# Performance work log

Hardware: AMD Instinct MI355X
Metric: run time of the kernel (lower is better)

## Reference

```python
import jax, jax.numpy as jnp
import numpy as np

B, T, N, F, H, E = 8, 24, 4000, 32, 128, 64000


def setup_inputs() -> dict:
    key = jax.random.key(0)
    ks = jax.random.split(key, 8)
    s = lambda k, shape: jax.random.normal(k, shape, jnp.float32) * 0.05
    return {
        "dynamic_features": jax.random.normal(ks[0], (B, T, N, F), jnp.float32),
        "edge_index": jax.random.randint(ks[1], (2, E), 0, N),
        "W_ih": s(ks[2], (4 * H, F)),
        "W_hh": s(ks[3], (4 * H, H)),
        "b_ih": jnp.zeros((4 * H,), jnp.float32),
        "b_hh": jnp.zeros((4 * H,), jnp.float32),
        "gcn_W": s(ks[4], (H, H)),
        "gcn_b": jnp.zeros((H,), jnp.float32),
        "fc_count_w": s(ks[5], (1, H)),
        "fc_count_b": jnp.zeros((1,), jnp.float32),
        "fc_income_w": s(ks[6], (1, H)),
        "fc_income_b": jnp.zeros((1,), jnp.float32),
    }


def _lstm_last(x, W_ih, W_hh, b_ih, b_hh):
    # x: [M, T, F] -> last hidden state [M, H]; PyTorch gate order (i, f, g, o)
    M = x.shape[0]
    Hh = W_hh.shape[1]
    xg = jnp.einsum('mtf,gf->mtg', x, W_ih) + b_ih + b_hh  # [M, T, 4H]

    def step(carry, xt):
        h, c = carry
        g = xt + h @ W_hh.T
        i, f, gg, o = jnp.split(g, 4, axis=-1)
        i = jax.nn.sigmoid(i)
        f = jax.nn.sigmoid(f)
        gg = jnp.tanh(gg)
        o = jax.nn.sigmoid(o)
        c = f * c + i * gg
        h = o * jnp.tanh(c)
        return (h, c), None

    h0 = jnp.zeros((M, Hh), x.dtype)
    (h, _), _ = jax.lax.scan(step, (h0, h0), jnp.swapaxes(xg, 0, 1))
    return h


def reference(dynamic_features, edge_index, W_ih, W_hh, b_ih, b_hh,
              gcn_W, gcn_b, fc_count_w, fc_count_b, fc_income_w, fc_income_b):
    b, t, n, f = dynamic_features.shape
    Hh = W_hh.shape[1]

    # temporal encoding: [B, T, N, F] -> [B*N, T, F] -> last hidden [B, N, H]
    lstm_in = dynamic_features.transpose(0, 2, 1, 3).reshape(b * n, t, f)
    h = _lstm_last(lstm_in, W_ih, W_hh, b_ih, b_hh).reshape(b, n, Hh)

    # PyG GCNConv norm: add self-loops, deg^{-1/2} on both ends
    loops = jnp.arange(n)
    src = jnp.concatenate([edge_index[0], loops])
    dst = jnp.concatenate([edge_index[1], loops])
    deg = jax.ops.segment_sum(jnp.ones_like(src, jnp.float32), dst, num_segments=n)
    dinv = jnp.where(deg > 0, deg ** -0.5, 0.0)
    norm = dinv[src] * dinv[dst]  # [E+N]

    def gcn_relu(xb):  # xb: [N, H]
        xw = xb @ gcn_W.T
        msg = xw[src] * norm[:, None]
        agg = jax.ops.segment_sum(msg, dst, num_segments=n) + gcn_b
        return jax.nn.relu(agg)

    gcn_out = jax.vmap(gcn_relu)(h)  # [B, N, H]

    count_pred = (gcn_out @ fc_count_w.T + fc_count_b).reshape(b, n)
    income_pred = (gcn_out @ fc_income_w.T + fc_income_b).reshape(b, n)
    return count_pred, income_pred
```

## Files before the change

kernel.cpp:

```cpp
#include <hip/hip_runtime.h>

#define NB 8
#define TT 24
#define NN 4000
#define FF 32
#define HH 128
#define EE 64000

typedef float f32x4 __attribute__((ext_vector_type(4)));
typedef short bf16x8 __attribute__((ext_vector_type(8)));
#define MFMA16(a, b, c) __builtin_amdgcn_mfma_f32_16x16x32_bf16(a, b, c, 0, 0, 0)

__device__ __forceinline__ float fsig(float x) {
  return __builtin_amdgcn_rcpf(1.0f + __expf(-x));
}
__device__ __forceinline__ float ftanh(float x) {
  return 1.0f - 2.0f * __builtin_amdgcn_rcpf(__expf(2.0f * x) + 1.0f);
}

__device__ __forceinline__ unsigned short rne16(float x, float* hif) {
  unsigned u = __float_as_uint(x);
  unsigned r = (u + 0x7FFFu + ((u >> 16) & 1u)) >> 16;
  *hif = __uint_as_float(r << 16);
  return (unsigned short)r;
}

__device__ __forceinline__ unsigned rnd_top(float x) {
  unsigned u = __float_as_uint(x);
  return u + 0x7FFFu + ((u >> 16) & 1u);
}

__global__ __launch_bounds__(256) void setup_xsplit_kernel(
    const float* __restrict__ x, const float* __restrict__ W_ih, const float* __restrict__ W_hh,
    const float* __restrict__ b_ih, const float* __restrict__ b_hh,
    const float* __restrict__ gcn_W,
    unsigned short* __restrict__ Wbh_hi, unsigned short* __restrict__ Wbh_lo,
    unsigned short* __restrict__ Wbi_hi, unsigned short* __restrict__ Wbi_lo,
    float* __restrict__ gcn_WT, float* __restrict__ bias,
    int* __restrict__ ecnt, int* __restrict__ fillc,
    unsigned short* __restrict__ xpk) {
  if (blockIdx.x < 418) {
    int idx = blockIdx.x * 256 + threadIdx.x;
    if (idx < 65536) {
      int e = idx & 7, l = (idx >> 3) & 63, ks = (idx >> 9) & 3, nt = idx >> 11;
      int gate = nt * 16 + (l & 15);
      int k = ks * 32 + (l >> 4) * 8 + e;
      float wv = W_hh[gate * 128 + k];
      float hif, d;
      unsigned short hb = rne16(wv, &hif);
      unsigned short lb = rne16(wv - hif, &d);
      Wbh_hi[idx] = hb;
      Wbh_lo[idx] = lb;
    } else if (idx < 65536 + 16384) {
      int p = idx - 65536;
      int e = p & 7, l = (p >> 3) & 63, nt = p >> 9;
      int gate = nt * 16 + (l & 15);
      int k = (l >> 4) * 8 + e;
      float wv = W_ih[gate * 32 + k];
      float hif, d;
      unsigned short hb = rne16(wv, &hif);
      unsigned short lb = rne16(wv - hif, &d);
      Wbi_hi[p] = hb;
      Wbi_lo[p] = lb;
    } else if (idx < 65536 + 16384 + 16384) {
      int p = idx - 65536 - 16384;
      int g = p & 127, k = p >> 7;
      gcn_WT[p] = gcn_W[g * 128 + k];
    } else if (idx < 65536 + 16384 + 16384 + 512) {
      int g = idx - (65536 + 16384 + 16384);
      bias[g] = b_ih[g] + b_hh[g];
    } else if (idx < 65536 + 16384 + 16384 + 512 + NN) {
      ecnt[idx - (65536 + 16384 + 16384 + 512)] = 0;
    } else if (idx < 65536 + 16384 + 16384 + 512 + 2 * NN) {
      fillc[idx - (65536 + 16384 + 16384 + 512 + NN)] = 0;
    }
  } else {
    int gid = (blockIdx.x - 418) * 256 + threadIdx.x;
    int l = gid & 63;
    int t = (gid >> 6) % TT;
    int rt = gid / (TT * 64);
    int col = l & 15, kc = l >> 4;
    int r = rt * 16 + col;
    int b = (rt * 16) / NN;
    int n = r - b * NN;
    const float* src = x + (((size_t)b * TT + t) * NN + n) * FF + kc * 8;
    float4 p0 = *(const float4*)src;
    float4 p1 = *(const float4*)(src + 4);
    float xf[8] = {p0.x, p0.y, p0.z, p0.w, p1.x, p1.y, p1.z, p1.w};
    bf16x8 vh, vl;
#pragma unroll
    for (int e = 0; e < 8; ++e) {
      float hif, d;
      vh[e] = (short)rne16(xf[e], &hif);
      vl[e] = (short)rne16(xf[e] - hif, &d);
    }
    size_t ob = (size_t)(rt * TT + t) * 1024 + l * 8;
    *(bf16x8*)(xpk + ob) = vh;
    *(bf16x8*)(xpk + ob + 512) = vl;
  }
}

__global__ __launch_bounds__(256) void lstm_kernel(
    const unsigned short* __restrict__ xpk,
    const unsigned short* __restrict__ Wbh_hi, const unsigned short* __restrict__ Wbh_lo,
    const unsigned short* __restrict__ Wbi_hi, const unsigned short* __restrict__ Wbi_lo,
    const float* __restrict__ bias,
    float* __restrict__ h_out) {
  __shared__ unsigned short hbuf[2][2][32 * 128];
  const int tid = threadIdx.x;
  const int w = tid >> 6, l = tid & 63;
  const int col = l & 15, kc = l >> 4;
  const int blk = blockIdx.x;

  {
    uint4* p0 = (uint4*)&hbuf[0][0][0];
    for (int i = tid; i < 1024; i += 256) p0[i] = make_uint4(0, 0, 0, 0);
  }

  float c[2][2][4];
#pragma unroll
  for (int sq = 0; sq < 2; ++sq)
#pragma unroll
    for (int u = 0; u < 2; ++u)
#pragma unroll
      for (int r = 0; r < 4; ++r) c[sq][u][r] = 0.0f;

  __syncthreads();

  for (int t = 0; t < TT; ++t) {
    const char* hr_hi = (const char*)&hbuf[t & 1][0][0];
    const char* hr_lo = (const char*)&hbuf[t & 1][1][0];
    char* hw_hi = (char*)&hbuf[(t + 1) & 1][0][0];
    char* hw_lo = (char*)&hbuf[(t + 1) & 1][1][0];

    bf16x8 xh[2], xl[2];
#pragma unroll
    for (int sq = 0; sq < 2; ++sq) {
      const unsigned short* xb = xpk + ((size_t)(blk * 2 + sq) * TT + t) * 1024 + l * 8;
      xh[sq] = *(const bf16x8*)xb;
      xl[sq] = *(const bf16x8*)(xb + 512);
    }

    f32x4 acc[2][8];

    __builtin_amdgcn_s_setprio(1);
#pragma unroll
    for (int ks = 0; ks < 4; ++ks) {
      bf16x8 bh[2], bl_[2];
#pragma unroll
      for (int sq = 0; sq < 2; ++sq) {
        int off = (16 * sq + col) * 256 + (((4 * ks + kc) ^ col) << 4);
        bh[sq] = *(const bf16x8*)(hr_hi + off);
        bl_[sq] = *(const bf16x8*)(hr_lo + off);
      }
#pragma unroll
      for (int q = 0; q < 8; ++q) {
        size_t wo = ((size_t)((4 * q + w) * 4 + ks) * 64 + l) * 8;
        bf16x8 wh = *(const bf16x8*)(Wbh_hi + wo);
        bf16x8 wl = *(const bf16x8*)(Wbh_lo + wo);
        f32x4 cseed;
        if (ks == 0)
          cseed = *(const f32x4*)(bias + (q >> 1) * 128 + ((q & 1) * 4 + w) * 16 + 4 * kc);
#pragma unroll
        for (int sq = 0; sq < 2; ++sq) {
          acc[sq][q] = MFMA16(wh, bh[sq], ks == 0 ? cseed : acc[sq][q]);
          acc[sq][q] = MFMA16(wh, bl_[sq], acc[sq][q]);
          acc[sq][q] = MFMA16(wl, bh[sq], acc[sq][q]);
        }
      }
    }
#pragma unroll
    for (int q = 0; q < 8; ++q) {
      size_t wo = ((size_t)(4 * q + w) * 64 + l) * 8;
      bf16x8 wh = *(const bf16x8*)(Wbi_hi + wo);
      bf16x8 wl = *(const bf16x8*)(Wbi_lo + wo);
#pragma unroll
      for (int sq = 0; sq < 2; ++sq) {
        acc[sq][q] = MFMA16(wh, xh[sq], acc[sq][q]);
        acc[sq][q] = MFMA16(wh, xl[sq], acc[sq][q]);
        acc[sq][q] = MFMA16(wl, xh[sq], acc[sq][q]);
      }
    }
    __builtin_amdgcn_s_setprio(0);

#pragma unroll
    for (int u = 0; u < 2; ++u) {
      int jb = w + 4 * u;
#pragma unroll
      for (int sq = 0; sq < 2; ++sq) {
        unsigned uh[4], ul[4];
        float hv[4];
#pragma unroll
        for (int r = 0; r < 4; ++r) {
          float iv = fsig(acc[sq][0 + u][r]);
          float fv = fsig(acc[sq][2 + u][r]);
          float gv = ftanh(acc[sq][4 + u][r]);
          float ov = fsig(acc[sq][6 + u][r]);
          float cc = fv * c[sq][u][r] + iv * gv;
          c[sq][u][r] = cc;
          float hh = ov * ftanh(cc);
          hv[r] = hh;
          unsigned uu = __float_as_uint(hh);
          uh[r] = uu;
          float hif = __uint_as_float(uu & 0xFFFF0000u);
          ul[r] = rnd_top(hh - hif);
        }
        uint2 phi, plo;
        phi.x = __builtin_amdgcn_perm(uh[1], uh[0], 0x07060302u);
        phi.y = __builtin_amdgcn_perm(uh[3], uh[2], 0x07060302u);
        plo.x = __builtin_amdgcn_perm(ul[1], ul[0], 0x07060302u);
        plo.y = __builtin_amdgcn_perm(ul[3], ul[2], 0x07060302u);
        int row = 16 * sq + col;
        int cs = (2 * jb + (kc >> 1)) ^ col;
        int woff = row * 256 + cs * 16 + 8 * (kc & 1);
        *(uint2*)(hw_hi + woff) = phi;
        *(uint2*)(hw_lo + woff) = plo;
        if (t == TT - 1) {
          int rowg = blk * 32 + 16 * sq + col;
          *(float4*)&h_out[(size_t)rowg * HH + 16 * jb + 4 * kc] =
              make_float4(hv[0], hv[1], hv[2], hv[3]);
        }
      }
    }
    __syncthreads();
  }
}

__global__ void hist_kernel(const int* __restrict__ ei, int* __restrict__ ecnt) {
  int e = blockIdx.x * 256 + threadIdx.x;
  if (e < EE) atomicAdd(&ecnt[ei[EE + e]], 1);
}

__global__ __launch_bounds__(1024) void scan_kernel(const int* __restrict__ ecnt,
                                                    int* __restrict__ rowptr,
                                                    float* __restrict__ dinv) {
  __shared__ int s[4096];
  int tid = threadIdx.x;
  for (int i = tid; i < 4096; i += 1024) {
    int v = (i < NN) ? ecnt[i] : 0;
    s[i] = v;
    if (i < NN) dinv[i] = 1.0f / sqrtf((float)v + 1.0f);
  }
  __syncthreads();
  for (int off = 1; off < 4096; off <<= 1) {
    int v[4];
#pragma unroll
    for (int k = 0; k < 4; ++k) {
      int i = tid + k * 1024;
      v[k] = s[i] + ((i >= off) ? s[i - off] : 0);
    }
    __syncthreads();
#pragma unroll
    for (int k = 0; k < 4; ++k) s[tid + k * 1024] = v[k];
    __syncthreads();
  }
  for (int i = tid; i <= NN; i += 1024) rowptr[i] = (i == 0) ? 0 : s[i - 1];
}

__global__ void fill_kernel(const int* __restrict__ ei, const float* __restrict__ dinv,
                            const int* __restrict__ rowptr, int* __restrict__ fillc,
                            int2* __restrict__ epk) {
  int e = blockIdx.x * 256 + threadIdx.x;
  if (e >= EE) return;
  int s = ei[e], d = ei[EE + e];
  int pos = rowptr[d] + atomicAdd(&fillc[d], 1);
  float nrm = dinv[s] * dinv[d];
  epk[pos] = make_int2(s, __float_as_int(nrm));
}

__global__ __launch_bounds__(128) void xw_kernel(const float* __restrict__ h,
                                                 const float* __restrict__ gcn_WT,
                                                 float* __restrict__ xw) {
  const int r0 = blockIdx.x * 8;
  const int g = threadIdx.x;
  __shared__ float hs[8][HH];
  for (int m = 0; m < 8; ++m) hs[m][g] = h[(size_t)(r0 + m) * HH + g];
  __syncthreads();
  float acc[8] = {0, 0, 0, 0, 0, 0, 0, 0};
#pragma unroll 4
  for (int k = 0; k < HH; ++k) {
    float w = gcn_WT[k * HH + g];
#pragma unroll
    for (int m = 0; m < 8; ++m) acc[m] += hs[m][k] * w;
  }
  for (int m = 0; m < 8; ++m) xw[(size_t)(r0 + m) * HH + g] = acc[m];
}

__global__ __launch_bounds__(128) void gather_final_kernel(
    const float* __restrict__ xw, const float* __restrict__ dinv,
    const int* __restrict__ rowptr, const int2* __restrict__ epk,
    const float* __restrict__ gcn_b,
    const float* __restrict__ fcw_c, const float* __restrict__ fcb_c,
    const float* __restrict__ fcw_i, const float* __restrict__ fcb_i,
    float* __restrict__ out) {
  const int d = blockIdx.x;
  const int j = threadIdx.x;
  float acc[NB];
#pragma unroll
  for (int b = 0; b < NB; ++b) acc[b] = 0.0f;
  const int p0 = rowptr[d], p1 = rowptr[d + 1];
  for (int p = p0; p < p1; ++p) {
    int2 ep = epk[p];
    int s = ep.x;
    float nrm = __int_as_float(ep.y);
#pragma unroll
    for (int b = 0; b < NB; ++b)
      acc[b] += xw[((size_t)b * NN + s) * HH + j] * nrm;
  }
  float sn = dinv[d] * dinv[d];
  float bj = gcn_b[j], wc = fcw_c[j], wi = fcw_i[j];
  __shared__ float red[2][NB][2];
  int lane = j & 63, wv = j >> 6;
#pragma unroll
  for (int b = 0; b < NB; ++b) {
    float v = acc[b] + xw[((size_t)b * NN + d) * HH + j] * sn + bj;
    v = fmaxf(v, 0.0f);
    float sc = v * wc, si = v * wi;
#pragma unroll
    for (int off = 32; off > 0; off >>= 1) {
      sc += __shfl_down(sc, off);
      si += __shfl_down(si, off);
    }
    if (lane == 0) {
      red[wv][b][0] = sc;
      red[wv][b][1] = si;
    }
  }
  __syncthreads();
  if (j < NB) {
    out[(size_t)j * NN + d] = red[0][j][0] + red[1][j][0] + fcb_c[0];
    out[(size_t)(NB + j) * NN + d] = red[0][j][1] + red[1][j][1] + fcb_i[0];
  }
}

extern "C" void kernel_launch(void* const* d_in, const int* in_sizes, int n_in,
                              void* d_out, int out_size, void* d_ws, size_t ws_size,
                              hipStream_t stream) {
  const float* x     = (const float*)d_in[0];
  const int*   ei    = (const int*)d_in[1];
  const float* W_ih  = (const float*)d_in[2];
  const float* W_hh  = (const float*)d_in[3];
  const float* b_ih  = (const float*)d_in[4];
  const float* b_hh  = (const float*)d_in[5];
  const float* gcn_W = (const float*)d_in[6];
  const float* gcn_b = (const float*)d_in[7];
  const float* fcw_c = (const float*)d_in[8];
  const float* fcb_c = (const float*)d_in[9];
  const float* fcw_i = (const float*)d_in[10];
  const float* fcb_i = (const float*)d_in[11];
  float* out = (float*)d_out;

  char* cur = (char*)d_ws;
  unsigned short* Wbh_hi = (unsigned short*)cur; cur += 65536 * 2;
  unsigned short* Wbh_lo = (unsigned short*)cur; cur += 65536 * 2;
  unsigned short* Wbi_hi = (unsigned short*)cur; cur += 16384 * 2;
  unsigned short* Wbi_lo = (unsigned short*)cur; cur += 16384 * 2;
  float* gcn_WT = (float*)cur; cur += 16384 * 4;
  float* bias   = (float*)cur; cur += 512 * 4;
  float* dinv   = (float*)cur; cur += 4096 * 4;
  int*   ecnt   = (int*)cur;   cur += 4096 * 4;
  int*   fillc  = (int*)cur;   cur += 4096 * 4;
  int*   rowptr = (int*)cur;   cur += 8192 * 4;
  int2*  epk    = (int2*)cur;  cur += (size_t)EE * 8;
  float* h_all  = (float*)cur; cur += (size_t)4096000 * 4;
  unsigned short* xpk = (unsigned short*)cur;
  float* xw = (float*)cur;

  setup_xsplit_kernel<<<12418, 256, 0, stream>>>(x, W_ih, W_hh, b_ih, b_hh, gcn_W,
                                                 Wbh_hi, Wbh_lo, Wbi_hi, Wbi_lo,
                                                 gcn_WT, bias, ecnt, fillc, xpk);
  lstm_kernel<<<(NB * NN) / 32, 256, 0, stream>>>(xpk, Wbh_hi, Wbh_lo, Wbi_hi, Wbi_lo,
                                                  bias, h_all);
  hist_kernel<<<EE / 256, 256, 0, stream>>>(ei, ecnt);
  scan_kernel<<<1, 1024, 0, stream>>>(ecnt, rowptr, dinv);
  fill_kernel<<<EE / 256, 256, 0, stream>>>(ei, dinv, rowptr, fillc, epk);
  xw_kernel<<<(NB * NN) / 8, 128, 0, stream>>>(h_all, gcn_WT, xw);
  gather_final_kernel<<<NN, 128, 0, stream>>>(xw, dinv, rowptr, epk, gcn_b,
                                              fcw_c, fcb_c, fcw_i, fcb_i, out);
}
```

Before: 461.6 us.

## Split LSTM gate accumulation into two halves and target two blocks per CU

The per-timestep gate GEMM is restructured so each wave computes accumulators for one half of its hidden columns (4 gate tiles) at a time, then applies the LSTM cell update before starting the other half, instead of holding all 8 tiles at once. This halves live accumulator registers, and launch_bounds now requests 2 blocks per CU to raise occupancy. The trade-off is reloading the h tile fragments from LDS twice per step and less MFMA back-to-back work per phase, in exchange for better latency hiding across waves.

```diff
diff --git a/kernel.cpp b/kernel.cpp
--- a/kernel.cpp
+++ b/kernel.cpp
@@ -100,7 +100,7 @@
   }
 }
 
-__global__ __launch_bounds__(256) void lstm_kernel(
+__global__ __launch_bounds__(256, 2) void lstm_kernel(
     const unsigned short* __restrict__ xpk,
     const unsigned short* __restrict__ Wbh_hi, const unsigned short* __restrict__ Wbh_lo,
     const unsigned short* __restrict__ Wbi_hi, const unsigned short* __restrict__ Wbi_lo,
@@ -141,50 +141,52 @@
       xl[sq] = *(const bf16x8*)(xb + 512);
     }
 
-    f32x4 acc[2][8];
-
-    __builtin_amdgcn_s_setprio(1);
-#pragma unroll
-    for (int ks = 0; ks < 4; ++ks) {
-      bf16x8 bh[2], bl_[2];
-#pragma unroll
-      for (int sq = 0; sq < 2; ++sq) {
-        int off = (16 * sq + col) * 256 + (((4 * ks + kc) ^ col) << 4);
-        bh[sq] = *(const bf16x8*)(hr_hi + off);
-        bl_[sq] = *(const bf16x8*)(hr_lo + off);
+#pragma unroll
+    for (int u = 0; u < 2; ++u) {
+      f32x4 acc[2][4];
+
+      __builtin_amdgcn_s_setprio(1);
+#pragma unroll
+      for (int ks = 0; ks < 4; ++ks) {
+        bf16x8 bh[2], bl_[2];
+#pragma unroll
+        for (int sq = 0; sq < 2; ++sq) {
+          int off = (16 * sq + col) * 256 + (((4 * ks + kc) ^ col) << 4);
+          bh[sq] = *(const bf16x8*)(hr_hi + off);
+          bl_[sq] = *(const bf16x8*)(hr_lo + off);
+        }
+#pragma unroll
+        for (int g = 0; g < 4; ++g) {
+          int nt = 8 * g + 4 * u + w;
+          size_t wo = ((size_t)(nt * 4 + ks) * 64 + l) * 8;
+          bf16x8 wh = *(const bf16x8*)(Wbh_hi + wo);
+          bf16x8 wl = *(const bf16x8*)(Wbh_lo + wo);
+          f32x4 cseed;
+          if (ks == 0)
+            cseed = *(const f32x4*)(bias + g * 128 + (4 * u + w) * 16 + 4 * kc);
+#pragma unroll
+          for (int sq = 0; sq < 2; ++sq) {
+            acc[sq][g] = MFMA16(wh, bh[sq], ks == 0 ? cseed : acc[sq][g]);
+            acc[sq][g] = MFMA16(wh, bl_[sq], acc[sq][g]);
+            acc[sq][g] = MFMA16(wl, bh[sq], acc[sq][g]);
+          }
+        }
       }
 #pragma unroll
-      for (int q = 0; q < 8; ++q) {
-        size_t wo = ((size_t)((4 * q + w) * 4 + ks) * 64 + l) * 8;
-        bf16x8 wh = *(const bf16x8*)(Wbh_hi + wo);
-        bf16x8 wl = *(const bf16x8*)(Wbh_lo + wo);
-        f32x4 cseed;
-        if (ks == 0)
-          cseed = *(const f32x4*)(bias + (q >> 1) * 128 + ((q & 1) * 4 + w) * 16 + 4 * kc);
+      for (int g = 0; g < 4; ++g) {
+        int nt = 8 * g + 4 * u + w;
+        size_t wo = ((size_t)nt * 64 + l) * 8;
+        bf16x8 wh = *(const bf16x8*)(Wbi_hi + wo);
+        bf16x8 wl = *(const bf16x8*)(Wbi_lo + wo);
 #pragma unroll
         for (int sq = 0; sq < 2; ++sq) {
-          acc[sq][q] = MFMA16(wh, bh[sq], ks == 0 ? cseed : acc[sq][q]);
-          acc[sq][q] = MFMA16(wh, bl_[sq], acc[sq][q]);
-          acc[sq][q] = MFMA16(wl, bh[sq], acc[sq][q]);
+          acc[sq][g] = MFMA16(wh, xh[sq], acc[sq][g]);
+          acc[sq][g] = MFMA16(wh, xl[sq], acc[sq][g]);
+          acc[sq][g] = MFMA16(wl, xh[sq], acc[sq][g]);
         }
       }
-    }
-#pragma unroll
-    for (int q = 0; q < 8; ++q) {
-      size_t wo = ((size_t)(4 * q + w) * 64 + l) * 8;
-      bf16x8 wh = *(const bf16x8*)(Wbi_hi + wo);
-      bf16x8 wl = *(const bf16x8*)(Wbi_lo + wo);
-#pragma unroll
-      for (int sq = 0; sq < 2; ++sq) {
-        acc[sq][q] = MFMA16(wh, xh[sq], acc[sq][q]);
-        acc[sq][q] = MFMA16(wh, xl[sq], acc[sq][q]);
-        acc[sq][q] = MFMA16(wl, xh[sq], acc[sq][q]);
-      }
-    }
-    __builtin_amdgcn_s_setprio(0);
-
-#pragma unroll
-    for (int u = 0; u < 2; ++u) {
+      __builtin_amdgcn_s_setprio(0);
+
       int jb = w + 4 * u;
 #pragma unroll
       for (int sq = 0; sq < 2; ++sq) {
@@ -192,10 +194,10 @@
         float hv[4];
 #pragma unroll
         for (int r = 0; r < 4; ++r) {
-          float iv = fsig(acc[sq][0 + u][r]);
-          float fv = fsig(acc[sq][2 + u][r]);
-          float gv = ftanh(acc[sq][4 + u][r]);
-          float ov = fsig(acc[sq][6 + u][r]);
+          float iv = fsig(acc[sq][0][r]);
+          float fv = fsig(acc[sq][1][r]);
+          float gv = ftanh(acc[sq][2][r]);
+          float ov = fsig(acc[sq][3][r]);
           float cc = fv * c[sq][u][r] + iv * gv;
           c[sq][u][r] = cc;
           float hh = ov * ftanh(cc);
```

Result: slower. 1.003 ms (+117.3%).

## Stream LSTM weight tiles into LDS with double-buffered async global_load_lds

Applied to the files above, without the earlier changes.

Replaces the per-step direct global loads of the recurrent and input weight fragments with a per-wave double-buffered prefetch pipeline. Each iteration uses global_load_lds to stage the next two gate tiles into LDS, waits with an explicit vmcnt, then reads the current tiles from LDS for the MFMAs. The aim is to hide L2 latency on weight fetches behind MFMA work. It also drops the s_setprio hints. It adds LDS traffic and extra waits, and the hand-written vmcnt depends on the compiler not reordering other global loads.

```diff
diff --git a/kernel.cpp b/kernel.cpp
--- a/kernel.cpp
+++ b/kernel.cpp
@@ -10,6 +10,10 @@
 typedef float f32x4 __attribute__((ext_vector_type(4)));
 typedef short bf16x8 __attribute__((ext_vector_type(8)));
 #define MFMA16(a, b, c) __builtin_amdgcn_mfma_f32_16x16x32_bf16(a, b, c, 0, 0, 0)
+
+typedef const __attribute__((address_space(1))) unsigned int* gas1_t;
+typedef __attribute__((address_space(3))) unsigned int* las3_t;
+#define DMA16(g, s) __builtin_amdgcn_global_load_lds((gas1_t)(g), (las3_t)(s), 16, 0, 0)
 
 __device__ __forceinline__ float fsig(float x) {
   return __builtin_amdgcn_rcpf(1.0f + __expf(-x));
@@ -107,6 +111,7 @@
     const float* __restrict__ bias,
     float* __restrict__ h_out) {
   __shared__ unsigned short hbuf[2][2][32 * 128];
+  __shared__ unsigned short wbuf[4][2][2048];
   const int tid = threadIdx.x;
   const int w = tid >> 6, l = tid & 63;
   const int col = l & 15, kc = l >> 4;
@@ -126,6 +131,14 @@
       for (int r = 0; r < 4; ++r) c[sq][u][r] = 0.0f;
 
   __syncthreads();
+
+#define HHOFF(q, ks) ((size_t)(((4 * (q) + w) * 4 + (ks)) * 512) + l * 8)
+#define IHOFF(q) ((size_t)((4 * (q) + w) * 512) + l * 8)
+
+  DMA16(Wbh_hi + HHOFF(0, 0), &wbuf[w][0][0]);
+  DMA16(Wbh_lo + HHOFF(0, 0), &wbuf[w][0][512]);
+  DMA16(Wbh_hi + HHOFF(1, 0), &wbuf[w][0][1024]);
+  DMA16(Wbh_lo + HHOFF(1, 0), &wbuf[w][0][1536]);
 
   for (int t = 0; t < TT; ++t) {
     const char* hr_hi = (const char*)&hbuf[t & 1][0][0];
@@ -143,7 +156,6 @@
 
     f32x4 acc[2][8];
 
-    __builtin_amdgcn_s_setprio(1);
 #pragma unroll
     for (int ks = 0; ks < 4; ++ks) {
       bf16x8 bh[2], bl_[2];
@@ -154,34 +166,79 @@
         bl_[sq] = *(const bf16x8*)(hr_lo + off);
       }
 #pragma unroll
-      for (int q = 0; q < 8; ++q) {
-        size_t wo = ((size_t)((4 * q + w) * 4 + ks) * 64 + l) * 8;
-        bf16x8 wh = *(const bf16x8*)(Wbh_hi + wo);
-        bf16x8 wl = *(const bf16x8*)(Wbh_lo + wo);
-        f32x4 cseed;
-        if (ks == 0)
-          cseed = *(const f32x4*)(bias + (q >> 1) * 128 + ((q & 1) * 4 + w) * 16 + 4 * kc);
+      for (int j = 0; j < 4; ++j) {
+        const int m = ks * 4 + j;
+        const int cpar = m & 1, npar = cpar ^ 1;
+        if (m + 1 < 16) {
+          const int nks = (m + 1) >> 2, nj = (m + 1) & 3;
+          const int nq0 = 2 * nj, nq1 = 2 * nj + 1;
+          DMA16(Wbh_hi + HHOFF(nq0, nks), &wbuf[w][npar][0]);
+          DMA16(Wbh_lo + HHOFF(nq0, nks), &wbuf[w][npar][512]);
+          DMA16(Wbh_hi + HHOFF(nq1, nks), &wbuf[w][npar][1024]);
+          DMA16(Wbh_lo + HHOFF(nq1, nks), &wbuf[w][npar][1536]);
+        } else {
+          DMA16(Wbi_hi + IHOFF(0), &wbuf[w][npar][0]);
+          DMA16(Wbi_lo + IHOFF(0), &wbuf[w][npar][512]);
+          DMA16(Wbi_hi + IHOFF(1), &wbuf[w][npar][1024]);
+          DMA16(Wbi_lo + IHOFF(1), &wbuf[w][npar][1536]);
+        }
+        asm volatile("s_waitcnt vmcnt(4)" ::: "memory");
+        const unsigned short* wb = &wbuf[w][cpar][0];
+        bf16x8 wh0 = *(const bf16x8*)(wb + l * 8);
+        bf16x8 wl0 = *(const bf16x8*)(wb + 512 + l * 8);
+        bf16x8 wh1 = *(const bf16x8*)(wb + 1024 + l * 8);
+        bf16x8 wl1 = *(const bf16x8*)(wb + 1536 + l * 8);
+        const int q0 = 2 * j, q1 = 2 * j + 1;
+        f32x4 cs0, cs1;
+        if (ks == 0) {
+          cs0 = *(const f32x4*)(bias + (q0 >> 1) * 128 + ((q0 & 1) * 4 + w) * 16 + 4 * kc);
+          cs1 = *(const f32x4*)(bias + (q1 >> 1) * 128 + ((q1 & 1) * 4 + w) * 16 + 4 * kc);
+        }
 #pragma unroll
         for (int sq = 0; sq < 2; ++sq) {
-          acc[sq][q] = MFMA16(wh, bh[sq], ks == 0 ? cseed : acc[sq][q]);
-          acc[sq][q] = MFMA16(wh, bl_[sq], acc[sq][q]);
-          acc[sq][q] = MFMA16(wl, bh[sq], acc[sq][q]);
+          acc[sq][q0] = MFMA16(wh0, bh[sq], ks == 0 ? cs0 : acc[sq][q0]);
+          acc[sq][q0] = MFMA16(wh0, bl_[sq], acc[sq][q0]);
+          acc[sq][q0] = MFMA16(wl0, bh[sq], acc[sq][q0]);
+          acc[sq][q1] = MFMA16(wh1, bh[sq], ks == 0 ? cs1 : acc[sq][q1]);
+          acc[sq][q1] = MFMA16(wh1, bl_[sq], acc[sq][q1]);
+          acc[sq][q1] = MFMA16(wl1, bh[sq], acc[sq][q1]);
         }
       }
     }
-#pragma unroll
-    for (int q = 0; q < 8; ++q) {
-      size_t wo = ((size_t)(4 * q + w) * 64 + l) * 8;
-      bf16x8 wh = *(const bf16x8*)(Wbi_hi + wo);
-      bf16x8 wl = *(const bf16x8*)(Wbi_lo + wo);
+
+#pragma unroll
+    for (int j = 0; j < 4; ++j) {
+      const int m = 16 + j;
+      const int cpar = m & 1, npar = cpar ^ 1;
+      if (j < 3) {
+        const int nq0 = 2 * (j + 1), nq1 = nq0 + 1;
+        DMA16(Wbi_hi + IHOFF(nq0), &wbuf[w][npar][0]);
+        DMA16(Wbi_lo + IHOFF(nq0), &wbuf[w][npar][512]);
+        DMA16(Wbi_hi + IHOFF(nq1), &wbuf[w][npar][1024]);
+        DMA16(Wbi_lo + IHOFF(nq1), &wbuf[w][npar][1536]);
+      } else {
+        DMA16(Wbh_hi + HHOFF(0, 0), &wbuf[w][npar][0]);
+        DMA16(Wbh_lo + HHOFF(0, 0), &wbuf[w][npar][512]);
+        DMA16(Wbh_hi + HHOFF(1, 0), &wbuf[w][npar][1024]);
+        DMA16(Wbh_lo + HHOFF(1, 0), &wbuf[w][npar][1536]);
+      }
+      asm volatile("s_waitcnt vmcnt(4)" ::: "memory");
+      const unsigned short* wb = &wbuf[w][cpar][0];
+      bf16x8 wh0 = *(const bf16x8*)(wb + l * 8);
+      bf16x8 wl0 = *(const bf16x8*)(wb + 512 + l * 8);
+      bf16x8 wh1 = *(const bf16x8*)(wb + 1024 + l * 8);
+      bf16x8 wl1 = *(const bf16x8*)(wb + 1536 + l * 8);
+      const int q0 = 2 * j, q1 = 2 * j + 1;
 #pragma unroll
       for (int sq = 0; sq < 2; ++sq) {
-        acc[sq][q] = MFMA16(wh, xh[sq], acc[sq][q]);
-        acc[sq][q] = MFMA16(wh, xl[sq], acc[sq][q]);
-        acc[sq][q] = MFMA16(wl, xh[sq], acc[sq][q]);
+        acc[sq][q0] = MFMA16(wh0, xh[sq], acc[sq][q0]);
+        acc[sq][q0] = MFMA16(wh0, xl[sq], acc[sq][q0]);
+        acc[sq][q0] = MFMA16(wl0, xh[sq], acc[sq][q0]);
+        acc[sq][q1] = MFMA16(wh1, xh[sq], acc[sq][q1]);
+        acc[sq][q1] = MFMA16(wh1, xl[sq], acc[sq][q1]);
+        acc[sq][q1] = MFMA16(wl1, xh[sq], acc[sq][q1]);
       }
     }
-    __builtin_amdgcn_s_setprio(0);
 
 #pragma unroll
     for (int u = 0; u < 2; ++u) {
@@ -224,6 +281,8 @@
     }
     __syncthreads();
   }
+#undef HHOFF
+#undef IHOFF
 }
 
 __global__ void hist_kernel(const int* __restrict__ ei, int* __restrict__ ecnt) {
```

After: 637.6 us. 38.1% more time.

## Stream LSTM weights through double-buffered LDS via async global_load_lds

Applied to the files above, without the earlier changes.

Replaces direct global loads of the recurrent and input weight fragments in the LSTM time loop with asynchronous global-to-LDS DMA copies, issued one phase ahead into a per-wave double buffer. Weights are consumed from LDS, and the wait is expressed as a manual vmcnt count. The goal is to hide global/L2 latency behind the MFMA work. In exchange it adds 64KB of LDS per block, which can cut occupancy, and drops the s_setprio hints. The hand-coded vmcnt accounting is fragile because the xpk and bias global loads share that counter.

```diff
diff --git a/kernel.cpp b/kernel.cpp
--- a/kernel.cpp
+++ b/kernel.cpp
@@ -10,6 +10,10 @@
 typedef float f32x4 __attribute__((ext_vector_type(4)));
 typedef short bf16x8 __attribute__((ext_vector_type(8)));
 #define MFMA16(a, b, c) __builtin_amdgcn_mfma_f32_16x16x32_bf16(a, b, c, 0, 0, 0)
+
+typedef const __attribute__((address_space(1))) unsigned int* gas1_t;
+typedef __attribute__((address_space(3))) unsigned int* las3_t;
+#define DMA16(g, s) __builtin_amdgcn_global_load_lds((gas1_t)(g), (las3_t)(s), 16, 0, 0)
 
 __device__ __forceinline__ float fsig(float x) {
   return __builtin_amdgcn_rcpf(1.0f + __expf(-x));
@@ -107,6 +111,7 @@
     const float* __restrict__ bias,
     float* __restrict__ h_out) {
   __shared__ unsigned short hbuf[2][2][32 * 128];
+  __shared__ unsigned short wbuf[4][2][8][512];
   const int tid = threadIdx.x;
   const int w = tid >> 6, l = tid & 63;
   const int col = l & 15, kc = l >> 4;
@@ -126,6 +131,25 @@
       for (int r = 0; r < 4; ++r) c[sq][u][r] = 0.0f;
 
   __syncthreads();
+
+#define STAGE(p, par)                                                              \
+  {                                                                                \
+    _Pragma("unroll") for (int s = 0; s < 8; ++s) {                                \
+      const unsigned short* srcp;                                                  \
+      if ((p) < 8) {                                                               \
+        int q = 4 * ((p) & 1) + (s >> 1);                                          \
+        size_t off = (size_t)(((4 * q + w) * 4 + ((p) >> 1)) * 512) + l * 8;       \
+        srcp = ((s & 1) ? Wbh_lo : Wbh_hi) + off;                                  \
+      } else {                                                                     \
+        int q = 4 * ((p) - 8) + (s >> 1);                                          \
+        size_t off = (size_t)((4 * q + w) * 512) + l * 8;                          \
+        srcp = ((s & 1) ? Wbi_lo : Wbi_hi) + off;                                  \
+      }                                                                            \
+      DMA16(srcp, &wbuf[w][par][s][0]);                                            \
+    }                                                                              \
+  }
+
+  STAGE(0, 0);
 
   for (int t = 0; t < TT; ++t) {
     const char* hr_hi = (const char*)&hbuf[t & 1][0][0];
@@ -133,55 +157,68 @@
     char* hw_hi = (char*)&hbuf[(t + 1) & 1][0][0];
     char* hw_lo = (char*)&hbuf[(t + 1) & 1][1][0];
 
+    f32x4 acc[2][8];
     bf16x8 xh[2], xl[2];
-#pragma unroll
-    for (int sq = 0; sq < 2; ++sq) {
-      const unsigned short* xb = xpk + ((size_t)(blk * 2 + sq) * TT + t) * 1024 + l * 8;
-      xh[sq] = *(const bf16x8*)xb;
-      xl[sq] = *(const bf16x8*)(xb + 512);
-    }
-
-    f32x4 acc[2][8];
-
-    __builtin_amdgcn_s_setprio(1);
-#pragma unroll
-    for (int ks = 0; ks < 4; ++ks) {
-      bf16x8 bh[2], bl_[2];
-#pragma unroll
-      for (int sq = 0; sq < 2; ++sq) {
-        int off = (16 * sq + col) * 256 + (((4 * ks + kc) ^ col) << 4);
-        bh[sq] = *(const bf16x8*)(hr_hi + off);
-        bl_[sq] = *(const bf16x8*)(hr_lo + off);
+
+#pragma unroll
+    for (int p = 0; p < 10; ++p) {
+      const int cpar = p & 1, npar = cpar ^ 1;
+      if (p < 9) {
+        STAGE(p + 1, npar);
+      } else {
+        STAGE(0, npar);
       }
-#pragma unroll
-      for (int q = 0; q < 8; ++q) {
-        size_t wo = ((size_t)((4 * q + w) * 4 + ks) * 64 + l) * 8;
-        bf16x8 wh = *(const bf16x8*)(Wbh_hi + wo);
-        bf16x8 wl = *(const bf16x8*)(Wbh_lo + wo);
-        f32x4 cseed;
-        if (ks == 0)
-          cseed = *(const f32x4*)(bias + (q >> 1) * 128 + ((q & 1) * 4 + w) * 16 + 4 * kc);
+      asm volatile("s_waitcnt vmcnt(8)" ::: "memory");
+
+      if (p == 0) {
 #pragma unroll
         for (int sq = 0; sq < 2; ++sq) {
-          acc[sq][q] = MFMA16(wh, bh[sq], ks == 0 ? cseed : acc[sq][q]);
-          acc[sq][q] = MFMA16(wh, bl_[sq], acc[sq][q]);
-          acc[sq][q] = MFMA16(wl, bh[sq], acc[sq][q]);
+          const unsigned short* xb = xpk + ((size_t)(blk * 2 + sq) * TT + t) * 1024 + l * 8;
+          xh[sq] = *(const bf16x8*)xb;
+          xl[sq] = *(const bf16x8*)(xb + 512);
         }
       }
-    }
-#pragma unroll
-    for (int q = 0; q < 8; ++q) {
-      size_t wo = ((size_t)(4 * q + w) * 64 + l) * 8;
-      bf16x8 wh = *(const bf16x8*)(Wbi_hi + wo);
-      bf16x8 wl = *(const bf16x8*)(Wbi_lo + wo);
-#pragma unroll
-      for (int sq = 0; sq < 2; ++sq) {
-        acc[sq][q] = MFMA16(wh, xh[sq], acc[sq][q]);
-        acc[sq][q] = MFMA16(wh, xl[sq], acc[sq][q]);
-        acc[sq][q] = MFMA16(wl, xh[sq], acc[sq][q]);
+
+      const unsigned short* wb = &wbuf[w][cpar][0][0];
+      if (p < 8) {
+        const int ks = p >> 1, h = p & 1;
+        bf16x8 bh[2], bl_[2];
+#pragma unroll
+        for (int sq = 0; sq < 2; ++sq) {
+          int off = (16 * sq + col) * 256 + (((4 * ks + kc) ^ col) << 4);
+          bh[sq] = *(const bf16x8*)(hr_hi + off);
+          bl_[sq] = *(const bf16x8*)(hr_lo + off);
+        }
+#pragma unroll
+        for (int j = 0; j < 4; ++j) {
+          const int q = 4 * h + j;
+          bf16x8 wh = *(const bf16x8*)(wb + (2 * j) * 512 + l * 8);
+          bf16x8 wl = *(const bf16x8*)(wb + (2 * j + 1) * 512 + l * 8);
+          f32x4 cseed;
+          if (ks == 0)
+            cseed = *(const f32x4*)(bias + (q >> 1) * 128 + ((q & 1) * 4 + w) * 16 + 4 * kc);
+#pragma unroll
+          for (int sq = 0; sq < 2; ++sq) {
+            acc[sq][q] = MFMA16(wh, bh[sq], ks == 0 ? cseed : acc[sq][q]);
+            acc[sq][q] = MFMA16(wh, bl_[sq], acc[sq][q]);
+            acc[sq][q] = MFMA16(wl, bh[sq], acc[sq][q]);
+          }
+        }
+      } else {
+#pragma unroll
+        for (int j = 0; j < 4; ++j) {
+          const int q = 4 * (p - 8) + j;
+          bf16x8 wh = *(const bf16x8*)(wb + (2 * j) * 512 + l * 8);
+          bf16x8 wl = *(const bf16x8*)(wb + (2 * j + 1) * 512 + l * 8);
+#pragma unroll
+          for (int sq = 0; sq < 2; ++sq) {
+            acc[sq][q] = MFMA16(wh, xh[sq], acc[sq][q]);
+            acc[sq][q] = MFMA16(wh, xl[sq], acc[sq][q]);
+            acc[sq][q] = MFMA16(wl, xh[sq], acc[sq][q]);
+          }
+        }
       }
     }
-    __builtin_amdgcn_s_setprio(0);
 
 #pragma unroll
     for (int u = 0; u < 2; ++u) {
@@ -224,6 +261,7 @@
     }
     __syncthreads();
   }
+#undef STAGE
 }
 
 __global__ void hist_kernel(const int* __restrict__ ei, int* __restrict__ ecnt) {
```

Result: slower. 694.3 us (+50.4%).
